# Kernel optimization log

Hardware: AMD Instinct MI355X
Metric: run time of the kernel (lower is better)

## Reference

```python
import jax, jax.numpy as jnp
import numpy as np

def setup_inputs() -> dict:
    key = jax.random.key(0)
    k1, k2 = jax.random.split(key)
    B, C, H, W = 8, 256, 96, 96
    fmap1 = jax.random.normal(k1, (B, C, H, W), dtype=jnp.float32)
    fmap2 = jax.random.normal(k2, (B, C, H, W), dtype=jnp.float32)
    return {"fmap1": fmap1, "fmap2": fmap2}

def reference(fmap1, fmap2):
    # Original: corr[b,i,j] = mean_{k,l} sum_c fmap1[b,c,i,j] * fmap2[b,c,k,l]
    # The spatial mean over fmap2 commutes with the channel contraction, so:
    #   corr = sum_c fmap1[b,c,i,j] * mean_{k,l} fmap2[b,c,k,l]
    # This avoids the O(H^2 W^2 C) bmm and the (B,H,W,H,W) intermediate.
    m2 = jnp.mean(fmap2, axis=(2, 3))                      # [B, C]
    corr = jnp.einsum('bchw,bc->bhw', fmap1, m2)           # [B, H, W]
    return corr[:, None, :, :]                             # [B, 1, H, W]
```

## Files before the change

kernel.cpp:

```cpp
#include <hip/hip_runtime.h>
#include <hip/hip_bf16.h>


#define B_ 8
#define C_ 256
#define HW_ 9216

__global__ __launch_bounds__(256) void mean2_kernel(const float* __restrict__ f2,
                                                    float* __restrict__ m2) {
    const int bc = blockIdx.x;
    const float4* p = (const float4*)(f2 + (size_t)bc * HW_);
    const int t = threadIdx.x;

    float s = 0.f;
#pragma unroll
    for (int k = 0; k < 9; ++k) {
        float4 v = p[t + k * 256];
        s += (v.x + v.y) + (v.z + v.w);
    }
#pragma unroll
    for (int off = 32; off > 0; off >>= 1)
        s += __shfl_down(s, off, 64);

    __shared__ float ws[4];
    const int wid = t >> 6, lane = t & 63;
    if (lane == 0) ws[wid] = s;
    __syncthreads();
    if (t == 0) {
        float tot = (ws[0] + ws[1]) + (ws[2] + ws[3]);
        m2[bc] = tot * (1.0f / (float)HW_);
    }
}

__global__ __launch_bounds__(256) void corr_kernel(const float* __restrict__ f1,
                                                   const float* __restrict__ m2,
                                                   float* __restrict__ out) {
    const int lin   = blockIdx.x;
    const int b     = lin / 72;
    const int rem   = lin % 72;
    const int hwblk = rem / 8;
    const int cblk  = rem % 8;
    const int c0    = cblk * 32;
    const int pos   = hwblk * 1024 + threadIdx.x * 4;

    const float* f1base = f1 + ((size_t)b * C_ + c0) * HW_ + pos;
    const float* m2base = m2 + b * C_ + c0;

    float4 acc = {0.f, 0.f, 0.f, 0.f};
#pragma unroll 8
    for (int i = 0; i < 32; ++i) {
        float  s = m2base[i];
        float4 v = *(const float4*)(f1base + (size_t)i * HW_);
        acc.x += v.x * s;
        acc.y += v.y * s;
        acc.z += v.z * s;
        acc.w += v.w * s;
    }

    float* o = out + (size_t)b * HW_ + pos;
    atomicAdd(o + 0, acc.x);
    atomicAdd(o + 1, acc.y);
    atomicAdd(o + 2, acc.z);
    atomicAdd(o + 3, acc.w);
}

extern "C" void kernel_launch(void* const* d_in, const int* in_sizes, int n_in,
                              void* d_out, int out_size, void* d_ws, size_t ws_size,
                              hipStream_t stream) {
    const float* f1 = (const float*)d_in[0];
    const float* f2 = (const float*)d_in[1];
    float* out = (float*)d_out;
    float* m2  = (float*)d_ws;

    hipMemsetAsync(d_out, 0, (size_t)out_size * sizeof(float), stream);

    mean2_kernel<<<B_ * C_, 256, 0, stream>>>(f2, m2);
    corr_kernel<<<576, 256, 0, stream>>>(f1, m2, out);
}
```

Measured before the change: 170.6 us.

## Fuse mean and correlation kernels into one launch with a grid-wide barrier

Replaces the two-kernel pipeline (plane means, then the channel-weighted sum) with one 576-block kernel. Each wave reduces a 1024-element slice of fmap2 and atomically adds it into a per-plane sum. An atomic-counter grid barrier then separates that phase from the correlation phase, which stages the 32 sums in shared memory and applies the 1/HW scaling at the end. The output zeroing moves into the kernel, and only the small workspace is memset, which removes one kernel launch and the large output memset. In exchange it relies on all 576 blocks being co-resident. If they are not, the spin-wait breaks on a timeout and would then read incomplete sums.

```diff
diff --git a/kernel.cpp b/kernel.cpp
--- a/kernel.cpp
+++ b/kernel.cpp
@@ -5,63 +5,84 @@
 #define B_ 8
 #define C_ 256
 #define HW_ 9216
+#define NPLANE (B_ * C_)
+#define GRID_ 576
 
-__global__ __launch_bounds__(256) void mean2_kernel(const float* __restrict__ f2,
-                                                    float* __restrict__ m2) {
-    const int bc = blockIdx.x;
-    const float4* p = (const float4*)(f2 + (size_t)bc * HW_);
-    const int t = threadIdx.x;
+__global__ __launch_bounds__(256, 4) void fused_kernel(const float* __restrict__ f1,
+                                                       const float* __restrict__ f2,
+                                                       float* __restrict__ m2sum,
+                                                       unsigned int* __restrict__ sem,
+                                                       float* __restrict__ out) {
+    const int t    = threadIdx.x;
+    const int bid  = blockIdx.x;
+    const int wave = t >> 6;
+    const int lane = t & 63;
 
-    float s = 0.f;
+    if (bid < 72) {
+        ((float4*)out)[bid * 256 + t] = make_float4(0.f, 0.f, 0.f, 0.f);
+    }
+
+#pragma unroll 4
+    for (int it = 0; it < 8; ++it) {
+        const int s   = bid * 32 + it * 4 + wave;
+        const int pp  = s / 9;
+        const int sub = s - pp * 9;
+        const float4* base = (const float4*)(f2 + (size_t)pp * HW_ + sub * 1024);
+        const float4 a = base[lane];
+        const float4 b = base[lane + 64];
+        const float4 c = base[lane + 128];
+        const float4 d = base[lane + 192];
+        float r = ((a.x + a.y) + (a.z + a.w)) + ((b.x + b.y) + (b.z + b.w))
+                + ((c.x + c.y) + (c.z + c.w)) + ((d.x + d.y) + (d.z + d.w));
 #pragma unroll
-    for (int k = 0; k < 9; ++k) {
-        float4 v = p[t + k * 256];
-        s += (v.x + v.y) + (v.z + v.w);
+        for (int off = 32; off; off >>= 1)
+            r += __shfl_down(r, off, 64);
+        if (lane == 0) atomicAdd(&m2sum[pp], r);
     }
-#pragma unroll
-    for (int off = 32; off > 0; off >>= 1)
-        s += __shfl_down(s, off, 64);
 
-    __shared__ float ws[4];
-    const int wid = t >> 6, lane = t & 63;
-    if (lane == 0) ws[wid] = s;
+    __threadfence();
     __syncthreads();
     if (t == 0) {
-        float tot = (ws[0] + ws[1]) + (ws[2] + ws[3]);
-        m2[bc] = tot * (1.0f / (float)HW_);
+        __hip_atomic_fetch_add(sem, 1u, __ATOMIC_RELEASE, __HIP_MEMORY_SCOPE_AGENT);
+        unsigned int spins = 0;
+        while (__hip_atomic_load(sem, __ATOMIC_ACQUIRE, __HIP_MEMORY_SCOPE_AGENT) < GRID_) {
+            __builtin_amdgcn_s_sleep(2);
+            if (++spins > (1u << 22)) break;
+        }
     }
-}
+    __syncthreads();
 
-__global__ __launch_bounds__(256) void corr_kernel(const float* __restrict__ f1,
-                                                   const float* __restrict__ m2,
-                                                   float* __restrict__ out) {
-    const int lin   = blockIdx.x;
-    const int b     = lin / 72;
-    const int rem   = lin % 72;
+    const int b     = bid / 72;
+    const int rem   = bid % 72;
     const int hwblk = rem / 8;
     const int cblk  = rem % 8;
     const int c0    = cblk * 32;
-    const int pos   = hwblk * 1024 + threadIdx.x * 4;
+    const int pos   = hwblk * 1024 + t * 4;
 
-    const float* f1base = f1 + ((size_t)b * C_ + c0) * HW_ + pos;
-    const float* m2base = m2 + b * C_ + c0;
+    __shared__ float sm2[32];
+    if (t < 32)
+        sm2[t] = __hip_atomic_load(&m2sum[b * C_ + c0 + t],
+                                   __ATOMIC_RELAXED, __HIP_MEMORY_SCOPE_AGENT);
+    __syncthreads();
 
+    const float* f1base = f1 + ((size_t)(b * C_ + c0)) * HW_ + pos;
     float4 acc = {0.f, 0.f, 0.f, 0.f};
-#pragma unroll 8
+#pragma unroll
     for (int i = 0; i < 32; ++i) {
-        float  s = m2base[i];
-        float4 v = *(const float4*)(f1base + (size_t)i * HW_);
-        acc.x += v.x * s;
-        acc.y += v.y * s;
-        acc.z += v.z * s;
-        acc.w += v.w * s;
+        const float  s = sm2[i];
+        const float4 w = *(const float4*)(f1base + (size_t)i * HW_);
+        acc.x += w.x * s;
+        acc.y += w.y * s;
+        acc.z += w.z * s;
+        acc.w += w.w * s;
     }
 
+    const float inv = 1.0f / (float)HW_;
     float* o = out + (size_t)b * HW_ + pos;
-    atomicAdd(o + 0, acc.x);
-    atomicAdd(o + 1, acc.y);
-    atomicAdd(o + 2, acc.z);
-    atomicAdd(o + 3, acc.w);
+    atomicAdd(o + 0, acc.x * inv);
+    atomicAdd(o + 1, acc.y * inv);
+    atomicAdd(o + 2, acc.z * inv);
+    atomicAdd(o + 3, acc.w * inv);
 }
 
 extern "C" void kernel_launch(void* const* d_in, const int* in_sizes, int n_in,
@@ -70,10 +91,10 @@
     const float* f1 = (const float*)d_in[0];
     const float* f2 = (const float*)d_in[1];
     float* out = (float*)d_out;
-    float* m2  = (float*)d_ws;
+    float* m2sum = (float*)d_ws;
+    unsigned int* sem = (unsigned int*)(m2sum + NPLANE);
 
-    hipMemsetAsync(d_out, 0, (size_t)out_size * sizeof(float), stream);
+    hipMemsetAsync(d_ws, 0, (NPLANE + 4) * sizeof(float), stream);
 
-    mean2_kernel<<<B_ * C_, 256, 0, stream>>>(f2, m2);
-    corr_kernel<<<576, 256, 0, stream>>>(f1, m2, out);
+    fused_kernel<<<GRID_, 256, 0, stream>>>(f1, f2, m2sum, sem, out);
 }
```

After: 304.1 us. 78.3% more time.

## Restructure corr kernel to reduce channels in-block and drop atomics and memset

Applied to the files above, without the earlier changes.

The corr kernel now gives each block 64 spatial positions of one batch and spreads the channels across its four waves. The partial sums are reduced through shared memory and written out directly, which removes the atomics and the memset launch. The per-batch means are staged in LDS. Loads change from float4 to scalar 256-byte coalesced rows, and each wave walks 64 channel planes, which may lower bytes in flight per load. The mean kernel now issues all of its loads before summing.

```diff
diff --git a/kernel.cpp b/kernel.cpp
--- a/kernel.cpp
+++ b/kernel.cpp
@@ -5,63 +5,59 @@
 #define B_ 8
 #define C_ 256
 #define HW_ 9216
+#define NPLANE (B_ * C_)
 
 __global__ __launch_bounds__(256) void mean2_kernel(const float* __restrict__ f2,
                                                     float* __restrict__ m2) {
     const int bc = blockIdx.x;
+    const int t  = threadIdx.x;
     const float4* p = (const float4*)(f2 + (size_t)bc * HW_);
-    const int t = threadIdx.x;
 
+    float4 v[9];
+#pragma unroll
+    for (int k = 0; k < 9; ++k) v[k] = p[t + k * 256];
     float s = 0.f;
 #pragma unroll
-    for (int k = 0; k < 9; ++k) {
-        float4 v = p[t + k * 256];
-        s += (v.x + v.y) + (v.z + v.w);
-    }
+    for (int k = 0; k < 9; ++k) s += (v[k].x + v[k].y) + (v[k].z + v[k].w);
+
 #pragma unroll
-    for (int off = 32; off > 0; off >>= 1)
-        s += __shfl_down(s, off, 64);
+    for (int off = 32; off; off >>= 1) s += __shfl_down(s, off, 64);
 
     __shared__ float ws[4];
-    const int wid = t >> 6, lane = t & 63;
-    if (lane == 0) ws[wid] = s;
+    if ((t & 63) == 0) ws[t >> 6] = s;
     __syncthreads();
-    if (t == 0) {
-        float tot = (ws[0] + ws[1]) + (ws[2] + ws[3]);
-        m2[bc] = tot * (1.0f / (float)HW_);
-    }
+    if (t == 0) m2[bc] = ((ws[0] + ws[1]) + (ws[2] + ws[3])) * (1.0f / (float)HW_);
 }
 
 __global__ __launch_bounds__(256) void corr_kernel(const float* __restrict__ f1,
                                                    const float* __restrict__ m2,
                                                    float* __restrict__ out) {
-    const int lin   = blockIdx.x;
-    const int b     = lin / 72;
-    const int rem   = lin % 72;
-    const int hwblk = rem / 8;
-    const int cblk  = rem % 8;
-    const int c0    = cblk * 32;
-    const int pos   = hwblk * 1024 + threadIdx.x * 4;
+    const int bid   = blockIdx.x;
+    const int b     = bid / 144;
+    const int chunk = bid % 144;
+    const int t     = threadIdx.x;
+    const int w     = t >> 6;
+    const int lane  = t & 63;
+    const int pos   = chunk * 64 + lane;
 
-    const float* f1base = f1 + ((size_t)b * C_ + c0) * HW_ + pos;
-    const float* m2base = m2 + b * C_ + c0;
+    __shared__ float sm2[C_];
+    sm2[t] = m2[b * C_ + t];
+    __syncthreads();
 
-    float4 acc = {0.f, 0.f, 0.f, 0.f};
+    const float* base = f1 + ((size_t)(b * C_ + w * 64)) * HW_ + pos;
+    float acc = 0.f;
 #pragma unroll 8
-    for (int i = 0; i < 32; ++i) {
-        float  s = m2base[i];
-        float4 v = *(const float4*)(f1base + (size_t)i * HW_);
-        acc.x += v.x * s;
-        acc.y += v.y * s;
-        acc.z += v.z * s;
-        acc.w += v.w * s;
+    for (int i = 0; i < 64; ++i) {
+        acc += sm2[w * 64 + i] * base[(size_t)i * HW_];
     }
 
-    float* o = out + (size_t)b * HW_ + pos;
-    atomicAdd(o + 0, acc.x);
-    atomicAdd(o + 1, acc.y);
-    atomicAdd(o + 2, acc.z);
-    atomicAdd(o + 3, acc.w);
+    __shared__ float part[256];
+    part[t] = acc;
+    __syncthreads();
+    if (t < 64) {
+        const float r = (part[t] + part[t + 64]) + (part[t + 128] + part[t + 192]);
+        out[(size_t)b * HW_ + chunk * 64 + t] = r;
+    }
 }
 
 extern "C" void kernel_launch(void* const* d_in, const int* in_sizes, int n_in,
@@ -72,8 +68,6 @@
     float* out = (float*)d_out;
     float* m2  = (float*)d_ws;
 
-    hipMemsetAsync(d_out, 0, (size_t)out_size * sizeof(float), stream);
-
-    mean2_kernel<<<B_ * C_, 256, 0, stream>>>(f2, m2);
-    corr_kernel<<<576, 256, 0, stream>>>(f1, m2, out);
+    mean2_kernel<<<NPLANE, 256, 0, stream>>>(f2, m2);
+    corr_kernel<<<1152, 256, 0, stream>>>(f1, m2, out);
 }
```

Result: no change. 169.2 us (-0.8%).
